# Kernel tuning notes

Measured on AMD Instinct MI355X. Metric: run time of the kernel, lower is better.

Reference implementation:

```python
import jax, jax.numpy as jnp
import numpy as np

F_DIM, H, O = 128, 256, 256
NQ, EQ = 64, 512
ND, ED = 50000, 600000

PARAM_SHAPES = [
    ("qW1", (F_DIM, H)), ("qb1", (H,)), ("qW2", (H, H)), ("qb2", (H,)),
    ("qW3", (H, H)),     ("qb3", (H,)), ("qW4", (H, O)), ("qb4", (O,)),
    ("dW1", (F_DIM, H)), ("db1", (H,)), ("dW2", (H, H)), ("db2", (H,)),
    ("dW3", (H, H)),     ("db3", (H,)), ("dW4", (H, O)), ("db4", (O,)),
    ("lW1", (2 * O, O)), ("lb1", (O,)),
    ("lW2", (O, O // 2)), ("lb2", (O // 2,)),
    ("lW3", (O // 2, 8)), ("lb3", (8,)),
]

def setup_inputs() -> dict:
    key = jax.random.key(0)
    ks = jax.random.split(key, 4 + len(PARAM_SHAPES))
    inp = {
        "query_in_feat": jax.random.normal(ks[0], (NQ, F_DIM), jnp.float32),
        "data_in_feat": jax.random.normal(ks[1], (ND, F_DIM), jnp.float32),
        "query_edge_list": jax.random.randint(ks[2], (2, EQ), 0, NQ),
        "data_edge_list": jax.random.randint(ks[3], (2, ED), 0, ND),
    }
    for i, (name, shape) in enumerate(PARAM_SHAPES):
        fan_in = shape[0] if len(shape) == 2 else 1
        inp[name] = jax.random.normal(ks[4 + i], shape, jnp.float32) * (1.0 / np.sqrt(fan_in))
    return inp

def _mlp2(x, W1, b1, W2, b2):
    return jnp.maximum(x @ W1 + b1, 0.0) @ W2 + b2

def _gin_conv(x, src, dst, W1, b1, W2, b2):
    # GINConv (eps=0): MLP(x_i + sum_{j->i} x_j); gather x[src], scatter-add at dst
    agg = jax.ops.segment_sum(x[src], dst, num_segments=x.shape[0])
    return _mlp2(x + agg, W1, b1, W2, b2)

def _gin(x, edge_index, p):
    src, dst = edge_index[0], edge_index[1]
    h = jnp.maximum(_gin_conv(x, src, dst, *p[:4]), 0.0)  # ReLU between convs
    return _gin_conv(h, src, dst, *p[4:])

def reference(query_in_feat, data_in_feat, query_edge_list, data_edge_list,
              qW1, qb1, qW2, qb2, qW3, qb3, qW4, qb4,
              dW1, db1, dW2, db2, dW3, db3, dW4, db4,
              lW1, lb1, lW2, lb2, lW3, lb3):
    qx = _gin(query_in_feat, query_edge_list, (qW1, qb1, qW2, qb2, qW3, qb3, qW4, qb4))
    dx = _gin(data_in_feat, data_edge_list, (dW1, db1, dW2, db2, dW3, db3, dW4, db4))
    # global_add_pool with batch = zeros -> single-graph sum
    qp = jnp.sum(qx, axis=0, keepdims=True)  # [1, O]
    dp = jnp.sum(dx, axis=0, keepdims=True)  # [1, O]
    h = jnp.concatenate([qp, dp], axis=1)    # [1, 2*O]
    h = jnp.maximum(h @ lW1 + lb1, 0.0)
    h = jnp.maximum(h @ lW2 + lb2, 0.0)
    h = jnp.maximum(h @ lW3 + lb3, 0.0)
    return h.reshape(1, 8)
```

## Files before the change

kernel.cpp:

```cpp
#include <hip/hip_runtime.h>
#include <hip/hip_bf16.h>


#define NQ 64
#define EQ 512
#define ND 50000
#define ED 600000
#define FDIM 128
#define HDIM 256

typedef __attribute__((ext_vector_type(8))) short short8;
typedef __attribute__((ext_vector_type(4))) float f32x4;
typedef __attribute__((ext_vector_type(2))) float floatx2;
typedef __attribute__((ext_vector_type(4))) unsigned short us4;
typedef __attribute__((ext_vector_type(2))) unsigned short us2;

__device__ __forceinline__ unsigned short f2bf(float f) {
    union { float f; unsigned u; } v; v.f = f;
    unsigned r = v.u + 0x7FFF + ((v.u >> 16) & 1);
    return (unsigned short)(r >> 16);
}
__device__ __forceinline__ float bf2f(unsigned short u) {
    union { unsigned u; float f; } v; v.u = ((unsigned)u) << 16;
    return v.f;
}


struct PackDesc {
    const float* W[8];
    unsigned short* Wp[8];
    int KT[8];
    int start[9];
};

__device__ __forceinline__ void pack_unit(const PackDesc& pd, int unit, int l) {
    int m = 0;
    while (m < 7 && unit >= pd.start[m + 1]) ++m;
    const int local = unit - pd.start[m];
    const int KT = pd.KT[m];
    const int kt = local % KT;
    const int ct = local / KT;
    const float* W = pd.W[m];
    unsigned short* Wp = pd.Wp[m];
    const int row = kt * 32 + (l >> 4) * 8;
    const int col = ct * 16 + (l & 15);
    short8 v;
#pragma unroll
    for (int j = 0; j < 8; ++j) v[j] = (short)f2bf(W[(size_t)(row + j) * 256 + col]);
    *(short8*)(Wp + (((size_t)(ct * KT + kt)) * 64 + l) * 8) = v;
}


__global__ void prepass(const float* __restrict__ xd, const float* __restrict__ xq,
                        unsigned char* __restrict__ x8, long long nd4, long long n4,
                        int cvt_b, PackDesc pd, int pack_units, int pack_b,
                        const int* __restrict__ d_dst, int* __restrict__ d_deg,
                        const int* __restrict__ q_dst, int* __restrict__ q_deg,
                        int d_eb) {
    const int b = blockIdx.x;
    const int tid = threadIdx.x;
    if (b < cvt_b) {
        long long i = (long long)b * 256 + tid;
        if (i >= n4) return;
        const float* src = (i < nd4) ? (xd + i * 4) : (xq + (i - nd4) * 4);
        float4 v = *(const float4*)src;
        int p = __builtin_amdgcn_cvt_pk_fp8_f32(v.x, v.y, 0, false);
        p = __builtin_amdgcn_cvt_pk_fp8_f32(v.z, v.w, p, true);
        *(unsigned*)(x8 + i * 4) = (unsigned)p;
    } else if (b < cvt_b + pack_b) {
        const int unit = (b - cvt_b) * 4 + (tid >> 6);
        if (unit < pack_units) pack_unit(pd, unit, tid & 63);
    } else {
        const int cb = b - cvt_b - pack_b;
        if (cb < d_eb) {
            int e = cb * 256 + tid;
            if (e < ED) atomicAdd(&d_deg[d_dst[e]], 1);
        } else {
            int e = (cb - d_eb) * 256 + tid;
            if (e < EQ) atomicAdd(&q_deg[q_dst[e]], 1);
        }
    }
}


__device__ __forceinline__ void scan1_body(const int* deg, int* rowptr, int* bsum,
                                           int n, int blk) {
    __shared__ int sh[256];
    const int t = threadIdx.x;
    const int i = blk * 256 + t;
    const int v = (i < n) ? deg[i] : 0;
    sh[t] = v;
    __syncthreads();
    for (int off = 1; off < 256; off <<= 1) {
        int x = (t >= off) ? sh[t - off] : 0;
        __syncthreads();
        sh[t] += x;
        __syncthreads();
    }
    if (i < n) rowptr[i] = sh[t] - v;
    if (t == 255) bsum[blk] = sh[255];
}

__global__ void scan_phase1_both(const int* __restrict__ d_deg, int* __restrict__ d_rowptr,
                                 int* __restrict__ d_bsum,
                                 const int* __restrict__ q_deg, int* __restrict__ q_rowptr,
                                 int* __restrict__ q_bsum, int dblocks) {
    int b = blockIdx.x;
    if (b < dblocks) scan1_body(d_deg, d_rowptr, d_bsum, ND, b);
    else             scan1_body(q_deg, q_rowptr, q_bsum, NQ, b - dblocks);
}

__device__ __forceinline__ void scan2_body(const int* bsum, int* boff, int* rowptr_n, int nb) {
    __shared__ int sh[256];
    const int t = threadIdx.x;
    const int v = (t < nb) ? bsum[t] : 0;
    sh[t] = v;
    __syncthreads();
    for (int off = 1; off < 256; off <<= 1) {
        int x = (t >= off) ? sh[t - off] : 0;
        __syncthreads();
        sh[t] += x;
        __syncthreads();
    }
    if (t < nb) boff[t] = sh[t] - v;
    if (t == 255) *rowptr_n = sh[255];
}

__global__ void scan_phase2_both(const int* __restrict__ d_bsum, int* __restrict__ d_boff,
                                 int* __restrict__ d_rowptr_n, int d_nb,
                                 const int* __restrict__ q_bsum, int* __restrict__ q_boff,
                                 int* __restrict__ q_rowptr_n, int q_nb) {
    if (blockIdx.x == 0) scan2_body(d_bsum, d_boff, d_rowptr_n, d_nb);
    else                 scan2_body(q_bsum, q_boff, q_rowptr_n, q_nb);
}

__global__ void scan_phase3_both(int* __restrict__ d_rowptr, const int* __restrict__ d_boff,
                                 int* __restrict__ d_cursor,
                                 int* __restrict__ q_rowptr, const int* __restrict__ q_boff,
                                 int* __restrict__ q_cursor, int dblocks) {
    int b = blockIdx.x;
    if (b < dblocks) {
        int i = b * 256 + threadIdx.x;
        if (i < ND) {
            int r = d_rowptr[i] + d_boff[b];
            d_rowptr[i] = r; d_cursor[i] = r;
        }
    } else {
        int i = (b - dblocks) * 256 + threadIdx.x;
        if (i < NQ) {
            int r = q_rowptr[i] + q_boff[b - dblocks];
            q_rowptr[i] = r; q_cursor[i] = r;
        }
    }
}

__global__ void fill_csr_both(const int* __restrict__ d_src, const int* __restrict__ d_dst,
                              int* __restrict__ d_cursor, int* __restrict__ d_csrsrc,
                              const int* __restrict__ q_src, const int* __restrict__ q_dst,
                              int* __restrict__ q_cursor, int* __restrict__ q_csrsrc,
                              int dblocks) {
    int b = blockIdx.x;
    if (b < dblocks) {
        int e = b * 256 + threadIdx.x;
        if (e < ED) {
            int p = atomicAdd(&d_cursor[d_dst[e]], 1);
            d_csrsrc[p] = d_src[e];
        }
    } else {
        int e = (b - dblocks) * 256 + threadIdx.x;
        if (e < EQ) {
            int p = atomicAdd(&q_cursor[q_dst[e]], 1);
            q_csrsrc[p] = q_src[e];
        }
    }
}


__global__ void gin_agg_f8_128_dual(const unsigned char* __restrict__ xd,
                                    const int* __restrict__ rpd, const int* __restrict__ csd,
                                    unsigned short* __restrict__ od,
                                    const unsigned char* __restrict__ xq,
                                    const int* __restrict__ rpq, const int* __restrict__ csq,
                                    unsigned short* __restrict__ oq, int ndpair) {
    const unsigned char* x; const int* rowptr; const int* csr; unsigned short* out; int nb;
    if ((int)blockIdx.x < ndpair) { x = xd; rowptr = rpd; csr = csd; out = od; nb = blockIdx.x; }
    else { x = xq; rowptr = rpq; csr = csq; out = oq; nb = blockIdx.x - ndpair; }

    const int t = threadIdx.x;
    const int node = nb * 2 + (t >> 5);
    const int c = t & 31;

    const int beg = rowptr[node];
    const int end = rowptr[node + 1];

    float a0, a1, a2, a3;
    {
        const unsigned w = *(const unsigned*)(x + (size_t)node * 128 + c * 4);
        floatx2 lo = __builtin_amdgcn_cvt_pk_f32_fp8((int)w, false);
        floatx2 hi = __builtin_amdgcn_cvt_pk_f32_fp8((int)w, true);
        a0 = lo[0]; a1 = lo[1]; a2 = hi[0]; a3 = hi[1];
    }
    for (int j = beg; j < end; ++j) {
        const unsigned w = *(const unsigned*)(x + (size_t)csr[j] * 128 + c * 4);
        floatx2 lo = __builtin_amdgcn_cvt_pk_f32_fp8((int)w, false);
        floatx2 hi = __builtin_amdgcn_cvt_pk_f32_fp8((int)w, true);
        a0 += lo[0]; a1 += lo[1]; a2 += hi[0]; a3 += hi[1];
    }
    us4 r;
    r[0] = f2bf(a0); r[1] = f2bf(a1); r[2] = f2bf(a2); r[3] = f2bf(a3);
    *(us4*)(out + (size_t)node * 128 + c * 4) = r;
}


__global__ void gin_agg_f8_256_dual(const unsigned char* __restrict__ xd,
                                    const int* __restrict__ rpd, const int* __restrict__ csd,
                                    unsigned short* __restrict__ od,
                                    const unsigned char* __restrict__ xq,
                                    const int* __restrict__ rpq, const int* __restrict__ csq,
                                    unsigned short* __restrict__ oq) {
    const unsigned char* x; const int* rowptr; const int* csr; unsigned short* out; int node;
    if ((int)blockIdx.x < ND) { x = xd; rowptr = rpd; csr = csd; out = od; node = blockIdx.x; }
    else { x = xq; rowptr = rpq; csr = csq; out = oq; node = blockIdx.x - ND; }

    const int t = threadIdx.x;
    const int beg = rowptr[node];
    const int end = rowptr[node + 1];

    float a0, a1, a2, a3;
    {
        const unsigned w = *(const unsigned*)(x + (size_t)node * 256 + t * 4);
        floatx2 lo = __builtin_amdgcn_cvt_pk_f32_fp8((int)w, false);
        floatx2 hi = __builtin_amdgcn_cvt_pk_f32_fp8((int)w, true);
        a0 = lo[0]; a1 = lo[1]; a2 = hi[0]; a3 = hi[1];
    }
    int j = beg;
    for (; j + 1 < end; j += 2) {
        const unsigned w0 = *(const unsigned*)(x + (size_t)csr[j] * 256 + t * 4);
        const unsigned w1 = *(const unsigned*)(x + (size_t)csr[j + 1] * 256 + t * 4);
        floatx2 l0 = __builtin_amdgcn_cvt_pk_f32_fp8((int)w0, false);
        floatx2 h0 = __builtin_amdgcn_cvt_pk_f32_fp8((int)w0, true);
        floatx2 l1 = __builtin_amdgcn_cvt_pk_f32_fp8((int)w1, false);
        floatx2 h1 = __builtin_amdgcn_cvt_pk_f32_fp8((int)w1, true);
        a0 += l0[0] + l1[0]; a1 += l0[1] + l1[1];
        a2 += h0[0] + h1[0]; a3 += h0[1] + h1[1];
    }
    if (j < end) {
        const unsigned w0 = *(const unsigned*)(x + (size_t)csr[j] * 256 + t * 4);
        floatx2 l0 = __builtin_amdgcn_cvt_pk_f32_fp8((int)w0, false);
        floatx2 h0 = __builtin_amdgcn_cvt_pk_f32_fp8((int)w0, true);
        a0 += l0[0]; a1 += l0[1]; a2 += h0[0]; a3 += h0[1];
    }
    us4 r;
    r[0] = f2bf(a0); r[1] = f2bf(a1); r[2] = f2bf(a2); r[3] = f2bf(a3);
    *(us4*)(out + (size_t)node * 256 + t * 4) = r;
}


template <int KIN>
__global__ __launch_bounds__(256) void mlp_dual(
    const unsigned short* __restrict__ Ad,
    const unsigned short* __restrict__ W1pd, const float* __restrict__ b1d,
    const unsigned short* __restrict__ W2pd, const float* __restrict__ b2d,
    unsigned char* __restrict__ C8d, float* __restrict__ poold, int nmb,
    const unsigned short* __restrict__ Aq,
    const unsigned short* __restrict__ W1pq, const float* __restrict__ b1q,
    const unsigned short* __restrict__ W2pq, const float* __restrict__ b2q,
    unsigned char* __restrict__ C8q, float* __restrict__ poolq,
    int relu_out) {
    constexpr int KT1 = KIN / 32;
    __shared__ __align__(16) unsigned short lds[32 * 256];

    const unsigned short* A; const unsigned short* W1p; const float* b1;
    const unsigned short* W2p; const float* b2;
    unsigned char* C8; float* pool; int row0, N;
    if ((int)blockIdx.x < nmb) {
        A = Ad; W1p = W1pd; b1 = b1d; W2p = W2pd; b2 = b2d;
        C8 = C8d; pool = poold; row0 = blockIdx.x * 32; N = ND;
    } else {
        A = Aq; W1p = W1pq; b1 = b1q; W2p = W2pq; b2 = b2q;
        C8 = C8q; pool = poolq; row0 = (blockIdx.x - nmb) * 32; N = NQ;
    }

    const int tid = threadIdx.x;
    const int lane = tid & 63;
    const int wv = tid >> 6;
    const int lrow = lane & 15;
    const int lk2 = (lane >> 4) * 8;
    const int nrows = (N - row0 < 32) ? (N - row0) : 32;

    for (int idx = tid; idx < nrows * (KIN / 8); idx += 256) {
        const int r = idx / (KIN / 8);
        const int k8 = (idx % (KIN / 8)) * 8;
        short8 v = *(const short8*)(A + (size_t)(row0 + r) * KIN + k8);
        unsigned byte = (unsigned)((r * KIN + k8) * 2) ^ (unsigned)((r & 7) << 4);
        *(short8*)((char*)lds + byte) = v;
    }
    __syncthreads();

    f32x4 acc1[2][4];
#pragma unroll
    for (int fm = 0; fm < 2; ++fm)
#pragma unroll
        for (int fn = 0; fn < 4; ++fn) acc1[fm][fn] = (f32x4)(0.f);

    const unsigned short* W1Base = W1p + ((size_t)(wv * 4) * KT1 * 64 + lane) * 8;
    for (int kt = 0; kt < KT1; ++kt) {
        short8 a[2], bf[4];
#pragma unroll
        for (int fm = 0; fm < 2; ++fm) {
            const int r = fm * 16 + lrow;
            unsigned byte = (unsigned)((r * KIN + kt * 32 + lk2) * 2) ^ (unsigned)((r & 7) << 4);
            a[fm] = *(const short8*)((const char*)lds + byte);
        }
#pragma unroll
        for (int fn = 0; fn < 4; ++fn)
            bf[fn] = *(const short8*)(W1Base + ((size_t)fn * KT1 + kt) * 64 * 8);
#pragma unroll
        for (int fm = 0; fm < 2; ++fm)
#pragma unroll
            for (int fn = 0; fn < 4; ++fn)
                acc1[fm][fn] = __builtin_amdgcn_mfma_f32_16x16x32_bf16(
                    a[fm], bf[fn], acc1[fm][fn], 0, 0, 0);
    }
    __syncthreads();

#pragma unroll
    for (int fn = 0; fn < 4; ++fn) {
        const int col = wv * 64 + fn * 16 + lrow;
        const float bv = b1[col];
#pragma unroll
        for (int fm = 0; fm < 2; ++fm) {
            const int rbase = fm * 16 + (lane >> 4) * 4;
#pragma unroll
            for (int r = 0; r < 4; ++r) {
                const int row = rbase + r;
                const float v = fmaxf(acc1[fm][fn][r] + bv, 0.f);
                unsigned byte = (unsigned)((row * 256 + col) * 2) ^ (unsigned)((row & 7) << 4);
                *(unsigned short*)((char*)lds + byte) = f2bf(v);
            }
        }
    }
    __syncthreads();

    f32x4 acc2[2][4];
#pragma unroll
    for (int fm = 0; fm < 2; ++fm)
#pragma unroll
        for (int fn = 0; fn < 4; ++fn) acc2[fm][fn] = (f32x4)(0.f);

    const unsigned short* W2Base = W2p + ((size_t)(wv * 4) * 8 * 64 + lane) * 8;
    for (int kt = 0; kt < 8; ++kt) {
        short8 a[2], bf[4];
#pragma unroll
        for (int fm = 0; fm < 2; ++fm) {
            const int r = fm * 16 + lrow;
            unsigned byte = (unsigned)((r * 256 + kt * 32 + lk2) * 2) ^ (unsigned)((r & 7) << 4);
            a[fm] = *(const short8*)((const char*)lds + byte);
        }
#pragma unroll
        for (int fn = 0; fn < 4; ++fn)
            bf[fn] = *(const short8*)(W2Base + ((size_t)fn * 8 + kt) * 64 * 8);
#pragma unroll
        for (int fm = 0; fm < 2; ++fm)
#pragma unroll
            for (int fn = 0; fn < 4; ++fn)
                acc2[fm][fn] = __builtin_amdgcn_mfma_f32_16x16x32_bf16(
                    a[fm], bf[fn], acc2[fm][fn], 0, 0, 0);
    }

#pragma unroll
    for (int fn = 0; fn < 4; ++fn) {
        const int col = wv * 64 + fn * 16 + lrow;
        const float bv = b2[col];
        float ps = 0.f;
#pragma unroll
        for (int fm = 0; fm < 2; ++fm) {
            const int rbase = row0 + fm * 16 + (lane >> 4) * 4;
#pragma unroll
            for (int r = 0; r < 4; ++r) {
                const int row = rbase + r;
                if (row < N) {
                    float v = acc2[fm][fn][r] + bv;
                    if (relu_out) v = fmaxf(v, 0.f);
                    if (C8) {
                        unsigned p = (unsigned)__builtin_amdgcn_cvt_pk_fp8_f32(v, v, 0, false);
                        C8[(size_t)row * 256 + col] = (unsigned char)(p & 0xff);
                    }
                    ps += v;
                }
            }
        }
        if (pool) {
            ps += __shfl_xor(ps, 16);
            ps += __shfl_xor(ps, 32);
            if ((lane >> 4) == 0) atomicAdd(&pool[col], ps);
        }
    }
}


__global__ void mlp_head(const float* __restrict__ pooled,
                         const float* __restrict__ lW1, const float* __restrict__ lb1,
                         const float* __restrict__ lW2, const float* __restrict__ lb2,
                         const float* __restrict__ lW3, const float* __restrict__ lb3,
                         float* __restrict__ out) {
    __shared__ float h0[512];
    __shared__ float h1[256];
    __shared__ float h2[128];
    const int t = threadIdx.x;
    h0[t] = pooled[t];
    h0[t + 256] = pooled[t + 256];
    __syncthreads();

    float acc = lb1[t];
    for (int k = 0; k < 512; ++k) acc += h0[k] * lW1[k * 256 + t];
    h1[t] = fmaxf(acc, 0.f);
    __syncthreads();

    if (t < 128) {
        float a = lb2[t];
        for (int k = 0; k < 256; ++k) a += h1[k] * lW2[k * 128 + t];
        h2[t] = fmaxf(a, 0.f);
    }
    __syncthreads();

    if (t < 8) {
        float a = lb3[t];
        for (int k = 0; k < 128; ++k) a += h2[k] * lW3[k * 8 + t];
        out[t] = fmaxf(a, 0.f);
    }
}


extern "C" void kernel_launch(void* const* d_in, const int* in_sizes, int n_in,
                              void* d_out, int out_size, void* d_ws, size_t ws_size,
                              hipStream_t stream) {
    const float* q_x  = (const float*)d_in[0];
    const float* d_x  = (const float*)d_in[1];
    const int*   q_el = (const int*)d_in[2];
    const int*   d_el = (const int*)d_in[3];
    const float* qW1 = (const float*)d_in[4];  const float* qb1 = (const float*)d_in[5];
    const float* qW2 = (const float*)d_in[6];  const float* qb2 = (const float*)d_in[7];
    const float* qW3 = (const float*)d_in[8];  const float* qb3 = (const float*)d_in[9];
    const float* qW4 = (const float*)d_in[10]; const float* qb4 = (const float*)d_in[11];
    const float* dW1 = (const float*)d_in[12]; const float* db1 = (const float*)d_in[13];
    const float* dW2 = (const float*)d_in[14]; const float* db2 = (const float*)d_in[15];
    const float* dW3 = (const float*)d_in[16]; const float* db3 = (const float*)d_in[17];
    const float* dW4 = (const float*)d_in[18]; const float* db4 = (const float*)d_in[19];
    const float* lW1 = (const float*)d_in[20]; const float* lb1 = (const float*)d_in[21];
    const float* lW2 = (const float*)d_in[22]; const float* lb2 = (const float*)d_in[23];
    const float* lW3 = (const float*)d_in[24]; const float* lb3 = (const float*)d_in[25];
    (void)in_sizes; (void)n_in; (void)out_size; (void)ws_size;

    const int* q_src = q_el;  const int* q_dst = q_el + EQ;
    const int* d_src = d_el;  const int* d_dst = d_el + ED;

    char* wsb = (char*)d_ws;
    size_t off = 0;
    auto alloc = [&](size_t bytes) { void* p = wsb + off; off += (bytes + 255) & ~(size_t)255; return p; };

    unsigned char*  x8d = (unsigned char*)alloc((size_t)ND * FDIM);
    unsigned char*  x8q = (unsigned char*)alloc((size_t)NQ * FDIM);
    unsigned short* dag = (unsigned short*)alloc((size_t)ND * FDIM * 2);
    unsigned short* qag = (unsigned short*)alloc((size_t)NQ * FDIM * 2);
    unsigned char*  h8d = (unsigned char*)alloc((size_t)ND * HDIM);
    unsigned char*  h8q = (unsigned char*)alloc((size_t)NQ * HDIM);
    unsigned short* had = (unsigned short*)alloc((size_t)ND * HDIM * 2);
    unsigned short* haq = (unsigned short*)alloc((size_t)NQ * HDIM * 2);
    float* pooled = (float*)alloc(512 * 4);
    int* d_deg    = (int*)alloc((size_t)ND * 4);
    int* q_deg    = (int*)alloc((size_t)NQ * 4);
    int* d_rowptr = (int*)alloc((size_t)(ND + 1) * 4);
    int* d_cursor = (int*)alloc((size_t)ND * 4);
    int* d_csrsrc = (int*)alloc((size_t)ED * 4);
    int* d_bsum   = (int*)alloc(256 * 4);
    int* d_boff   = (int*)alloc(256 * 4);
    int* q_rowptr = (int*)alloc((size_t)(NQ + 1) * 4);
    int* q_cursor = (int*)alloc((size_t)NQ * 4);
    int* q_csrsrc = (int*)alloc((size_t)EQ * 4);
    int* q_bsum   = (int*)alloc(256 * 4);
    int* q_boff   = (int*)alloc(256 * 4);
    unsigned short* pdW1 = (unsigned short*)alloc((size_t)FDIM * 256 * 2);
    unsigned short* pdW2 = (unsigned short*)alloc((size_t)HDIM * 256 * 2);
    unsigned short* pdW3 = (unsigned short*)alloc((size_t)HDIM * 256 * 2);
    unsigned short* pdW4 = (unsigned short*)alloc((size_t)HDIM * 256 * 2);
    unsigned short* pqW1 = (unsigned short*)alloc((size_t)FDIM * 256 * 2);
    unsigned short* pqW2 = (unsigned short*)alloc((size_t)HDIM * 256 * 2);
    unsigned short* pqW3 = (unsigned short*)alloc((size_t)HDIM * 256 * 2);
    unsigned short* pqW4 = (unsigned short*)alloc((size_t)HDIM * 256 * 2);

    hipMemsetAsync(pooled, 0, 512 * 4, stream);
    hipMemsetAsync(d_deg, 0, (char*)(q_deg + NQ) - (char*)d_deg, stream);

    const int d_eb = (ED + 255) / 256;
    const int q_eb = (EQ + 255) / 256;
    const int d_nb = (ND + 255) / 256;
    const int q_nb = (NQ + 255) / 256;
    {
        PackDesc pd;
        const float* Ws[8] = {dW1, dW2, dW3, dW4, qW1, qW2, qW3, qW4};
        unsigned short* Wps[8] = {pdW1, pdW2, pdW3, pdW4, pqW1, pqW2, pqW3, pqW4};
        int kts[8] = {4, 8, 8, 8, 4, 8, 8, 8};
        int s = 0;
        for (int i = 0; i < 8; ++i) {
            pd.W[i] = Ws[i]; pd.Wp[i] = Wps[i]; pd.KT[i] = kts[i];
            pd.start[i] = s; s += 16 * kts[i];
        }
        pd.start[8] = s;
        const int pack_units = s;
        const int pack_b = (s + 3) / 4;
        long long nd4 = (long long)ND * FDIM / 4;
        long long n4 = nd4 + (long long)NQ * FDIM / 4;
        const int cvt_b = (int)((n4 + 255) / 256);
        prepass<<<cvt_b + pack_b + d_eb + q_eb, 256, 0, stream>>>(
            d_x, q_x, x8d, nd4, n4, cvt_b, pd, pack_units, pack_b,
            d_dst, d_deg, q_dst, q_deg, d_eb);
    }

    scan_phase1_both<<<d_nb + q_nb, 256, 0, stream>>>(d_deg, d_rowptr, d_bsum,
                                                      q_deg, q_rowptr, q_bsum, d_nb);
    scan_phase2_both<<<2, 256, 0, stream>>>(d_bsum, d_boff, d_rowptr + ND, d_nb,
                                            q_bsum, q_boff, q_rowptr + NQ, q_nb);
    scan_phase3_both<<<d_nb + q_nb, 256, 0, stream>>>(d_rowptr, d_boff, d_cursor,
                                                      q_rowptr, q_boff, q_cursor, d_nb);
    fill_csr_both<<<d_eb + q_eb, 256, 0, stream>>>(d_src, d_dst, d_cursor, d_csrsrc,
                                                   q_src, q_dst, q_cursor, q_csrsrc, d_eb);

    const int ndpair = ND / 2;
    const int qpair = NQ / 2;
    const int nmb = (ND + 31) / 32;
    const int qmb = (NQ + 31) / 32;

    gin_agg_f8_128_dual<<<ndpair + qpair, 64, 0, stream>>>(
        x8d, d_rowptr, d_csrsrc, dag, x8q, q_rowptr, q_csrsrc, qag, ndpair);
    mlp_dual<FDIM><<<nmb + qmb, 256, 0, stream>>>(
        dag, pdW1, db1, pdW2, db2, h8d, nullptr, nmb,
        qag, pqW1, qb1, pqW2, qb2, h8q, nullptr, 1);

    gin_agg_f8_256_dual<<<ND + NQ, 64, 0, stream>>>(
        h8d, d_rowptr, d_csrsrc, had, h8q, q_rowptr, q_csrsrc, haq);
    mlp_dual<HDIM><<<nmb + qmb, 256, 0, stream>>>(
        had, pdW3, db3, pdW4, db4, nullptr, pooled + 256, nmb,
        haq, pqW3, qb3, pqW4, qb4, nullptr, pooled, 0);

    mlp_head<<<1, 256, 0, stream>>>(pooled, lW1, lb1, lW2, lb2, lW3, lb3, (float*)d_out);
}
```

Before: 251.7 us.

## Make MLP kernel persistent with 64-row tiles and double-buffered async LDS staging

```diff
diff --git a/kernel.cpp b/kernel.cpp
--- a/kernel.cpp
+++ b/kernel.cpp
@@ -8,6 +8,7 @@
 #define ED 600000
 #define FDIM 128
 #define HDIM 256
+#define MLP_GRID 512
 
 typedef __attribute__((ext_vector_type(8))) short short8;
 typedef __attribute__((ext_vector_type(4))) float f32x4;
@@ -261,140 +262,162 @@
     const unsigned short* __restrict__ Ad,
     const unsigned short* __restrict__ W1pd, const float* __restrict__ b1d,
     const unsigned short* __restrict__ W2pd, const float* __restrict__ b2d,
-    unsigned char* __restrict__ C8d, float* __restrict__ poold, int nmb,
+    unsigned char* __restrict__ C8d, float* __restrict__ poold, int ndtiles,
     const unsigned short* __restrict__ Aq,
     const unsigned short* __restrict__ W1pq, const float* __restrict__ b1q,
     const unsigned short* __restrict__ W2pq, const float* __restrict__ b2q,
     unsigned char* __restrict__ C8q, float* __restrict__ poolq,
-    int relu_out) {
+    int relu_out, int total_tiles) {
     constexpr int KT1 = KIN / 32;
-    __shared__ __align__(16) unsigned short lds[32 * 256];
-
-    const unsigned short* A; const unsigned short* W1p; const float* b1;
-    const unsigned short* W2p; const float* b2;
-    unsigned char* C8; float* pool; int row0, N;
-    if ((int)blockIdx.x < nmb) {
-        A = Ad; W1p = W1pd; b1 = b1d; W2p = W2pd; b2 = b2d;
-        C8 = C8d; pool = poold; row0 = blockIdx.x * 32; N = ND;
-    } else {
-        A = Aq; W1p = W1pq; b1 = b1q; W2p = W2pq; b2 = b2q;
-        C8 = C8q; pool = poolq; row0 = (blockIdx.x - nmb) * 32; N = NQ;
-    }
+    constexpr int ISSUES = KIN / 32;
+    constexpr int LPR = KIN / 8;
+    constexpr int RPC = 1024 / (2 * KIN);
+    __shared__ __align__(16) unsigned short lds[2][64 * 256];
 
     const int tid = threadIdx.x;
     const int lane = tid & 63;
     const int wv = tid >> 6;
     const int lrow = lane & 15;
     const int lk2 = (lane >> 4) * 8;
-    const int nrows = (N - row0 < 32) ? (N - row0) : 32;
-
-    for (int idx = tid; idx < nrows * (KIN / 8); idx += 256) {
-        const int r = idx / (KIN / 8);
-        const int k8 = (idx % (KIN / 8)) * 8;
-        short8 v = *(const short8*)(A + (size_t)(row0 + r) * KIN + k8);
-        unsigned byte = (unsigned)((r * KIN + k8) * 2) ^ (unsigned)((r & 7) << 4);
-        *(short8*)((char*)lds + byte) = v;
-    }
-    __syncthreads();
-
-    f32x4 acc1[2][4];
-#pragma unroll
-    for (int fm = 0; fm < 2; ++fm)
-#pragma unroll
-        for (int fn = 0; fn < 4; ++fn) acc1[fm][fn] = (f32x4)(0.f);
-
-    const unsigned short* W1Base = W1p + ((size_t)(wv * 4) * KT1 * 64 + lane) * 8;
-    for (int kt = 0; kt < KT1; ++kt) {
-        short8 a[2], bf[4];
-#pragma unroll
-        for (int fm = 0; fm < 2; ++fm) {
-            const int r = fm * 16 + lrow;
-            unsigned byte = (unsigned)((r * KIN + kt * 32 + lk2) * 2) ^ (unsigned)((r & 7) << 4);
-            a[fm] = *(const short8*)((const char*)lds + byte);
-        }
-#pragma unroll
-        for (int fn = 0; fn < 4; ++fn)
-            bf[fn] = *(const short8*)(W1Base + ((size_t)fn * KT1 + kt) * 64 * 8);
-#pragma unroll
-        for (int fm = 0; fm < 2; ++fm)
+
+    const int nt = (total_tiles - (int)blockIdx.x + MLP_GRID - 1) / MLP_GRID;
+    if (nt <= 0) return;
+
+    const int rc = lane / LPR;
+    const int cc = lane % LPR;
+
+    auto STAGE = [&](int bu, int g) {
+        const unsigned short* Abase =
+            (g < ndtiles) ? (Ad + (size_t)g * 64 * KIN) : (Aq + (size_t)(g - ndtiles) * 64 * KIN);
+#pragma unroll
+        for (int i = 0; i < ISSUES; ++i) {
+            const int chunk = wv * ISSUES + i;
+            const int r = chunk * RPC + rc;
+            const char* src = (const char*)Abase + (size_t)r * (2 * KIN) + ((cc ^ (r & 7)) << 4);
+            __builtin_amdgcn_global_load_lds(src, (char*)&lds[bu][0] + chunk * 1024, 16, 0, 0);
+        }
+    };
+
+    STAGE(0, (int)blockIdx.x);
+    int cur = 0;
+
+    for (int t = 0; t < nt; ++t) {
+        const int g = (int)blockIdx.x + t * MLP_GRID;
+        const unsigned short *W1p, *W2p; const float *b1, *b2;
+        unsigned char* C8; float* pool; int row0, N;
+        if (g < ndtiles) {
+            W1p = W1pd; b1 = b1d; W2p = W2pd; b2 = b2d; C8 = C8d; pool = poold;
+            row0 = g * 64; N = ND;
+        } else {
+            W1p = W1pq; b1 = b1q; W2p = W2pq; b2 = b2q; C8 = C8q; pool = poolq;
+            row0 = (g - ndtiles) * 64; N = NQ;
+        }
+
+        __syncthreads();
+        if (t + 1 < nt) STAGE(cur ^ 1, (int)blockIdx.x + (t + 1) * MLP_GRID);
+
+        unsigned short* buf = &lds[cur][0];
+
+        f32x4 acc1[4][4];
+#pragma unroll
+        for (int fm = 0; fm < 4; ++fm)
+#pragma unroll
+            for (int fn = 0; fn < 4; ++fn) acc1[fm][fn] = (f32x4)(0.f);
+
+        const unsigned short* W1Base = W1p + ((size_t)(wv * 4) * KT1 * 64 + lane) * 8;
+        for (int kt = 0; kt < KT1; ++kt) {
+            short8 a[4], bf[4];
+#pragma unroll
+            for (int fm = 0; fm < 4; ++fm) {
+                const int r = fm * 16 + lrow;
+                unsigned byte = (unsigned)((r * KIN + kt * 32 + lk2) * 2) ^ (unsigned)((r & 7) << 4);
+                a[fm] = *(const short8*)((const char*)buf + byte);
+            }
 #pragma unroll
             for (int fn = 0; fn < 4; ++fn)
-                acc1[fm][fn] = __builtin_amdgcn_mfma_f32_16x16x32_bf16(
-                    a[fm], bf[fn], acc1[fm][fn], 0, 0, 0);
-    }
-    __syncthreads();
-
-#pragma unroll
-    for (int fn = 0; fn < 4; ++fn) {
-        const int col = wv * 64 + fn * 16 + lrow;
-        const float bv = b1[col];
-#pragma unroll
-        for (int fm = 0; fm < 2; ++fm) {
-            const int rbase = fm * 16 + (lane >> 4) * 4;
-#pragma unroll
-            for (int r = 0; r < 4; ++r) {
-                const int row = rbase + r;
-                const float v = fmaxf(acc1[fm][fn][r] + bv, 0.f);
-                unsigned byte = (unsigned)((row * 256 + col) * 2) ^ (unsigned)((row & 7) << 4);
-                *(unsigned short*)((char*)lds + byte) = f2bf(v);
-            }
-        }
-    }
-    __syncthreads();
-
-    f32x4 acc2[2][4];
-#pragma unroll
-    for (int fm = 0; fm < 2; ++fm)
-#pragma unroll
-        for (int fn = 0; fn < 4; ++fn) acc2[fm][fn] = (f32x4)(0.f);
-
-    const unsigned short* W2Base = W2p + ((size_t)(wv * 4) * 8 * 64 + lane) * 8;
-    for (int kt = 0; kt < 8; ++kt) {
-        short8 a[2], bf[4];
-#pragma unroll
-        for (int fm = 0; fm < 2; ++fm) {
-            const int r = fm * 16 + lrow;
-            unsigned byte = (unsigned)((r * 256 + kt * 32 + lk2) * 2) ^ (unsigned)((r & 7) << 4);
-            a[fm] = *(const short8*)((const char*)lds + byte);
-        }
-#pragma unroll
-        for (int fn = 0; fn < 4; ++fn)
-            bf[fn] = *(const short8*)(W2Base + ((size_t)fn * 8 + kt) * 64 * 8);
-#pragma unroll
-        for (int fm = 0; fm < 2; ++fm)
-#pragma unroll
-            for (int fn = 0; fn < 4; ++fn)
-                acc2[fm][fn] = __builtin_amdgcn_mfma_f32_16x16x32_bf16(
-                    a[fm], bf[fn], acc2[fm][fn], 0, 0, 0);
-    }
-
-#pragma unroll
-    for (int fn = 0; fn < 4; ++fn) {
-        const int col = wv * 64 + fn * 16 + lrow;
-        const float bv = b2[col];
-        float ps = 0.f;
-#pragma unroll
-        for (int fm = 0; fm < 2; ++fm) {
-            const int rbase = row0 + fm * 16 + (lane >> 4) * 4;
-#pragma unroll
-            for (int r = 0; r < 4; ++r) {
-                const int row = rbase + r;
-                if (row < N) {
-                    float v = acc2[fm][fn][r] + bv;
-                    if (relu_out) v = fmaxf(v, 0.f);
-                    if (C8) {
-                        unsigned p = (unsigned)__builtin_amdgcn_cvt_pk_fp8_f32(v, v, 0, false);
-                        C8[(size_t)row * 256 + col] = (unsigned char)(p & 0xff);
-                    }
-                    ps += v;
+                bf[fn] = *(const short8*)(W1Base + ((size_t)fn * KT1 + kt) * 64 * 8);
+#pragma unroll
+            for (int fm = 0; fm < 4; ++fm)
+#pragma unroll
+                for (int fn = 0; fn < 4; ++fn)
+                    acc1[fm][fn] = __builtin_amdgcn_mfma_f32_16x16x32_bf16(
+                        a[fm], bf[fn], acc1[fm][fn], 0, 0, 0);
+        }
+        __syncthreads();
+
+#pragma unroll
+        for (int fn = 0; fn < 4; ++fn) {
+            const int col = wv * 64 + fn * 16 + lrow;
+            const float bv = b1[col];
+#pragma unroll
+            for (int fm = 0; fm < 4; ++fm) {
+                const int rbase = fm * 16 + (lane >> 4) * 4;
+#pragma unroll
+                for (int r = 0; r < 4; ++r) {
+                    const int row = rbase + r;
+                    const float v = fmaxf(acc1[fm][fn][r] + bv, 0.f);
+                    unsigned byte = (unsigned)((row * 256 + col) * 2) ^ (unsigned)((row & 7) << 4);
+                    *(unsigned short*)((char*)buf + byte) = f2bf(v);
                 }
             }
         }
-        if (pool) {
-            ps += __shfl_xor(ps, 16);
-            ps += __shfl_xor(ps, 32);
-            if ((lane >> 4) == 0) atomicAdd(&pool[col], ps);
-        }
+        __syncthreads();
+
+        f32x4 acc2[4][4];
+#pragma unroll
+        for (int fm = 0; fm < 4; ++fm)
+#pragma unroll
+            for (int fn = 0; fn < 4; ++fn) acc2[fm][fn] = (f32x4)(0.f);
+
+        const unsigned short* W2Base = W2p + ((size_t)(wv * 4) * 8 * 64 + lane) * 8;
+        for (int kt = 0; kt < 8; ++kt) {
+            short8 a[4], bf[4];
+#pragma unroll
+            for (int fm = 0; fm < 4; ++fm) {
+                const int r = fm * 16 + lrow;
+                unsigned byte = (unsigned)((r * 256 + kt * 32 + lk2) * 2) ^ (unsigned)((r & 7) << 4);
+                a[fm] = *(const short8*)((const char*)buf + byte);
+            }
+#pragma unroll
+            for (int fn = 0; fn < 4; ++fn)
+                bf[fn] = *(const short8*)(W2Base + ((size_t)fn * 8 + kt) * 64 * 8);
+#pragma unroll
+            for (int fm = 0; fm < 4; ++fm)
+#pragma unroll
+                for (int fn = 0; fn < 4; ++fn)
+                    acc2[fm][fn] = __builtin_amdgcn_mfma_f32_16x16x32_bf16(
+                        a[fm], bf[fn], acc2[fm][fn], 0, 0, 0);
+        }
+
+#pragma unroll
+        for (int fn = 0; fn < 4; ++fn) {
+            const int col = wv * 64 + fn * 16 + lrow;
+            const float bv = b2[col];
+            float ps = 0.f;
+#pragma unroll
+            for (int fm = 0; fm < 4; ++fm) {
+                const int rbase = row0 + fm * 16 + (lane >> 4) * 4;
+#pragma unroll
+                for (int r = 0; r < 4; ++r) {
+                    const int row = rbase + r;
+                    if (row < N) {
+                        float v = acc2[fm][fn][r] + bv;
+                        if (relu_out) v = fmaxf(v, 0.f);
+                        if (C8) {
+                            unsigned p = (unsigned)__builtin_amdgcn_cvt_pk_fp8_f32(v, v, 0, false);
+                            C8[(size_t)row * 256 + col] = (unsigned char)(p & 0xff);
+                        }
+                        ps += v;
+                    }
+                }
+            }
+            if (pool) {
+                ps += __shfl_xor(ps, 16);
+                ps += __shfl_xor(ps, 32);
+                if ((lane >> 4) == 0) atomicAdd(&pool[col], ps);
+            }
+        }
+        cur ^= 1;
     }
 }
 
@@ -528,20 +551,20 @@
 
     const int ndpair = ND / 2;
     const int qpair = NQ / 2;
-    const int nmb = (ND + 31) / 32;
-    const int qmb = (NQ + 31) / 32;
+    const int ndtiles = (ND + 63) / 64;
+    const int total_tiles = ndtiles + 1;
 
     gin_agg_f8_128_dual<<<ndpair + qpair, 64, 0, stream>>>(
         x8d, d_rowptr, d_csrsrc, dag, x8q, q_rowptr, q_csrsrc, qag, ndpair);
-    mlp_dual<FDIM><<<nmb + qmb, 256, 0, stream>>>(
-        dag, pdW1, db1, pdW2, db2, h8d, nullptr, nmb,
-        qag, pqW1, qb1, pqW2, qb2, h8q, nullptr, 1);
+    mlp_dual<FDIM><<<MLP_GRID, 256, 0, stream>>>(
+        dag, pdW1, db1, pdW2, db2, h8d, nullptr, ndtiles,
+        qag, pqW1, qb1, pqW2, qb2, h8q, nullptr, 1, total_tiles);
 
     gin_agg_f8_256_dual<<<ND + NQ, 64, 0, stream>>>(
         h8d, d_rowptr, d_csrsrc, had, h8q, q_rowptr, q_csrsrc, haq);
-    mlp_dual<HDIM><<<nmb + qmb, 256, 0, stream>>>(
-        had, pdW3, db3, pdW4, db4, nullptr, pooled + 256, nmb,
-        haq, pqW3, qb3, pqW4, qb4, nullptr, pooled, 0);
+    mlp_dual<HDIM><<<MLP_GRID, 256, 0, stream>>>(
+        had, pdW3, db3, pdW4, db4, nullptr, pooled + 256, ndtiles,
+        haq, pqW3, qb3, pqW4, qb4, nullptr, pooled, 0, total_tiles);
 
     mlp_head<<<1, 256, 0, stream>>>(pooled, lW1, lb1, lW2, lb2, lW3, lb3, (float*)d_out);
 }
```

Measured after the change: 272.5 us. 1.08x slower.

## Double MLP row tile to 64 and load layer-1 A fragments from global

Applied to the files above, without the earlier changes.

```diff
diff --git a/kernel.cpp b/kernel.cpp
--- a/kernel.cpp
+++ b/kernel.cpp
@@ -261,24 +261,24 @@
     const unsigned short* __restrict__ Ad,
     const unsigned short* __restrict__ W1pd, const float* __restrict__ b1d,
     const unsigned short* __restrict__ W2pd, const float* __restrict__ b2d,
-    unsigned char* __restrict__ C8d, float* __restrict__ poold, int nmb,
+    unsigned char* __restrict__ C8d, float* __restrict__ poold, int ndb,
     const unsigned short* __restrict__ Aq,
     const unsigned short* __restrict__ W1pq, const float* __restrict__ b1q,
     const unsigned short* __restrict__ W2pq, const float* __restrict__ b2q,
     unsigned char* __restrict__ C8q, float* __restrict__ poolq,
     int relu_out) {
     constexpr int KT1 = KIN / 32;
-    __shared__ __align__(16) unsigned short lds[32 * 256];
+    __shared__ __align__(16) unsigned short lds[64 * 256];
 
     const unsigned short* A; const unsigned short* W1p; const float* b1;
     const unsigned short* W2p; const float* b2;
     unsigned char* C8; float* pool; int row0, N;
-    if ((int)blockIdx.x < nmb) {
+    if ((int)blockIdx.x < ndb) {
         A = Ad; W1p = W1pd; b1 = b1d; W2p = W2pd; b2 = b2d;
-        C8 = C8d; pool = poold; row0 = blockIdx.x * 32; N = ND;
+        C8 = C8d; pool = poold; row0 = blockIdx.x * 64; N = ND;
     } else {
         A = Aq; W1p = W1pq; b1 = b1q; W2p = W2pq; b2 = b2q;
-        C8 = C8q; pool = poolq; row0 = (blockIdx.x - nmb) * 32; N = NQ;
+        C8 = C8q; pool = poolq; row0 = 0; N = NQ;
     }
 
     const int tid = threadIdx.x;
@@ -286,50 +286,39 @@
     const int wv = tid >> 6;
     const int lrow = lane & 15;
     const int lk2 = (lane >> 4) * 8;
-    const int nrows = (N - row0 < 32) ? (N - row0) : 32;
-
-    for (int idx = tid; idx < nrows * (KIN / 8); idx += 256) {
-        const int r = idx / (KIN / 8);
-        const int k8 = (idx % (KIN / 8)) * 8;
-        short8 v = *(const short8*)(A + (size_t)(row0 + r) * KIN + k8);
-        unsigned byte = (unsigned)((r * KIN + k8) * 2) ^ (unsigned)((r & 7) << 4);
-        *(short8*)((char*)lds + byte) = v;
-    }
-    __syncthreads();
-
-    f32x4 acc1[2][4];
-#pragma unroll
-    for (int fm = 0; fm < 2; ++fm)
+
+    f32x4 acc1[4][4];
+#pragma unroll
+    for (int fm = 0; fm < 4; ++fm)
 #pragma unroll
         for (int fn = 0; fn < 4; ++fn) acc1[fm][fn] = (f32x4)(0.f);
 
     const unsigned short* W1Base = W1p + ((size_t)(wv * 4) * KT1 * 64 + lane) * 8;
+    const unsigned short* Alane = A + (size_t)(row0 + lrow) * KIN + lk2;
+
+#pragma unroll
     for (int kt = 0; kt < KT1; ++kt) {
-        short8 a[2], bf[4];
-#pragma unroll
-        for (int fm = 0; fm < 2; ++fm) {
-            const int r = fm * 16 + lrow;
-            unsigned byte = (unsigned)((r * KIN + kt * 32 + lk2) * 2) ^ (unsigned)((r & 7) << 4);
-            a[fm] = *(const short8*)((const char*)lds + byte);
-        }
+        short8 a[4], bf[4];
+#pragma unroll
+        for (int fm = 0; fm < 4; ++fm)
+            a[fm] = *(const short8*)(Alane + (size_t)(fm * 16) * KIN + kt * 32);
 #pragma unroll
         for (int fn = 0; fn < 4; ++fn)
             bf[fn] = *(const short8*)(W1Base + ((size_t)fn * KT1 + kt) * 64 * 8);
 #pragma unroll
-        for (int fm = 0; fm < 2; ++fm)
+        for (int fm = 0; fm < 4; ++fm)
 #pragma unroll
             for (int fn = 0; fn < 4; ++fn)
                 acc1[fm][fn] = __builtin_amdgcn_mfma_f32_16x16x32_bf16(
                     a[fm], bf[fn], acc1[fm][fn], 0, 0, 0);
     }
-    __syncthreads();
 
 #pragma unroll
     for (int fn = 0; fn < 4; ++fn) {
         const int col = wv * 64 + fn * 16 + lrow;
         const float bv = b1[col];
 #pragma unroll
-        for (int fm = 0; fm < 2; ++fm) {
+        for (int fm = 0; fm < 4; ++fm) {
             const int rbase = fm * 16 + (lane >> 4) * 4;
 #pragma unroll
             for (int r = 0; r < 4; ++r) {
@@ -342,17 +331,18 @@
     }
     __syncthreads();
 
-    f32x4 acc2[2][4];
-#pragma unroll
-    for (int fm = 0; fm < 2; ++fm)
+    f32x4 acc2[4][4];
+#pragma unroll
+    for (int fm = 0; fm < 4; ++fm)
 #pragma unroll
         for (int fn = 0; fn < 4; ++fn) acc2[fm][fn] = (f32x4)(0.f);
 
     const unsigned short* W2Base = W2p + ((size_t)(wv * 4) * 8 * 64 + lane) * 8;
+#pragma unroll
     for (int kt = 0; kt < 8; ++kt) {
-        short8 a[2], bf[4];
-#pragma unroll
-        for (int fm = 0; fm < 2; ++fm) {
+        short8 a[4], bf[4];
+#pragma unroll
+        for (int fm = 0; fm < 4; ++fm) {
             const int r = fm * 16 + lrow;
             unsigned byte = (unsigned)((r * 256 + kt * 32 + lk2) * 2) ^ (unsigned)((r & 7) << 4);
             a[fm] = *(const short8*)((const char*)lds + byte);
@@ -361,7 +351,7 @@
         for (int fn = 0; fn < 4; ++fn)
             bf[fn] = *(const short8*)(W2Base + ((size_t)fn * 8 + kt) * 64 * 8);
 #pragma unroll
-        for (int fm = 0; fm < 2; ++fm)
+        for (int fm = 0; fm < 4; ++fm)
 #pragma unroll
             for (int fn = 0; fn < 4; ++fn)
                 acc2[fm][fn] = __builtin_amdgcn_mfma_f32_16x16x32_bf16(
@@ -374,7 +364,7 @@
         const float bv = b2[col];
         float ps = 0.f;
 #pragma unroll
-        for (int fm = 0; fm < 2; ++fm) {
+        for (int fm = 0; fm < 4; ++fm) {
             const int rbase = row0 + fm * 16 + (lane >> 4) * 4;
 #pragma unroll
             for (int r = 0; r < 4; ++r) {
@@ -462,11 +452,11 @@
     unsigned char*  x8d = (unsigned char*)alloc((size_t)ND * FDIM);
     unsigned char*  x8q = (unsigned char*)alloc((size_t)NQ * FDIM);
     unsigned short* dag = (unsigned short*)alloc((size_t)ND * FDIM * 2);
-    unsigned short* qag = (unsigned short*)alloc((size_t)NQ * FDIM * 2);
+    unsigned short* qag = (unsigned short*)alloc((size_t)(NQ + 64) * FDIM * 2);
     unsigned char*  h8d = (unsigned char*)alloc((size_t)ND * HDIM);
     unsigned char*  h8q = (unsigned char*)alloc((size_t)NQ * HDIM);
     unsigned short* had = (unsigned short*)alloc((size_t)ND * HDIM * 2);
-    unsigned short* haq = (unsigned short*)alloc((size_t)NQ * HDIM * 2);
+    unsigned short* haq = (unsigned short*)alloc((size_t)(NQ + 64) * HDIM * 2);
     float* pooled = (float*)alloc(512 * 4);
     int* d_deg    = (int*)alloc((size_t)ND * 4);
     int* q_deg    = (int*)alloc((size_t)NQ * 4);
@@ -528,19 +518,18 @@
 
     const int ndpair = ND / 2;
     const int qpair = NQ / 2;
-    const int nmb = (ND + 31) / 32;
-    const int qmb = (NQ + 31) / 32;
+    const int ndb = (ND + 63) / 64;
 
     gin_agg_f8_128_dual<<<ndpair + qpair, 64, 0, stream>>>(
         x8d, d_rowptr, d_csrsrc, dag, x8q, q_rowptr, q_csrsrc, qag, ndpair);
-    mlp_dual<FDIM><<<nmb + qmb, 256, 0, stream>>>(
-        dag, pdW1, db1, pdW2, db2, h8d, nullptr, nmb,
+    mlp_dual<FDIM><<<ndb + 1, 256, 0, stream>>>(
+        dag, pdW1, db1, pdW2, db2, h8d, nullptr, ndb,
         qag, pqW1, qb1, pqW2, qb2, h8q, nullptr, 1);
 
     gin_agg_f8_256_dual<<<ND + NQ, 64, 0, stream>>>(
         h8d, d_rowptr, d_csrsrc, had, h8q, q_rowptr, q_csrsrc, haq);
-    mlp_dual<HDIM><<<nmb + qmb, 256, 0, stream>>>(
-        had, pdW3, db3, pdW4, db4, nullptr, pooled + 256, nmb,
+    mlp_dual<HDIM><<<ndb + 1, 256, 0, stream>>>(
+        had, pdW3, db3, pdW4, db4, nullptr, pooled + 256, ndb,
         haq, pqW3, qb3, pqW4, qb4, nullptr, pooled, 0);
 
     mlp_head<<<1, 256, 0, stream>>>(pooled, lW1, lb1, lW2, lb2, lW3, lb3, (float*)d_out);
```

New measurement: 256.1 us. No clear change (+1.8%).
